# Kernel optimization log

Measured on AMD Instinct MI355X. Metric: run time of the kernel, lower is better.

## Reference

```python
import jax, jax.numpy as jnp
import numpy as np

SEQ, BSZ = 512, 128
VOC, EMB, HDIM = 50000, 128, 256
TAGS = 7
BOS, EOS, PAD = 4, 5, 6
H = HDIM // 2  # per-direction hidden size
NEG = -10000.0


def setup_inputs() -> dict:
    key = jax.random.key(0)
    ks = jax.random.split(key, 12)
    s = 0.08  # ~ pytorch default init scale for these sizes
    trans = jax.random.normal(ks[10], (TAGS, TAGS), dtype=jnp.float32)
    # constraints applied in __init__: no transition FROM BOS targets / INTO EOS etc.
    trans = trans.at[BOS, :].set(NEG).at[:, EOS].set(NEG).at[PAD, :].set(0.0)
    return {
        "sen": jax.random.randint(ks[0], (SEQ, BSZ), 0, VOC),                # (S, B) token ids
        "emb": jax.random.normal(ks[1], (VOC, EMB), jnp.float32) * s,        # embedding table
        "Wih_f": jax.random.normal(ks[2], (4 * H, EMB), jnp.float32) * s,    # fwd dir, gates i,f,g,o
        "Whh_f": jax.random.normal(ks[3], (4 * H, H), jnp.float32) * s,
        "b_f": jax.random.normal(ks[4], (4 * H,), jnp.float32) * s,          # b_ih + b_hh fused
        "Wih_b": jax.random.normal(ks[5], (4 * H, EMB), jnp.float32) * s,    # bwd dir
        "Whh_b": jax.random.normal(ks[6], (4 * H, H), jnp.float32) * s,
        "b_b": jax.random.normal(ks[7], (4 * H,), jnp.float32) * s,
        "W_out": jax.random.normal(ks[8], (TAGS, HDIM), jnp.float32) * s,    # hid2tag
        "b_out": jax.random.normal(ks[9], (TAGS,), jnp.float32) * s,
        "trans": trans,                                                      # trans[next, prev]
    }


def _lstm_dir(x, Wih, Whh, b, reverse):
    """Single-direction LSTM over (S, B, E) -> (S, B, H). PyTorch gate order i,f,g,o."""
    xw = jnp.einsum('sbe,ge->sbg', x, Wih) + b  # hoist input projection out of scan

    def step(carry, xt):
        h, c = carry
        g = xt + h @ Whh.T
        i, f, gg, o = jnp.split(g, 4, axis=-1)
        c = jax.nn.sigmoid(f) * c + jax.nn.sigmoid(i) * jnp.tanh(gg)
        h = jax.nn.sigmoid(o) * jnp.tanh(c)
        return (h, c), h

    B = x.shape[1]
    h0 = jnp.zeros((B, H), x.dtype)
    _, hs = jax.lax.scan(step, (h0, h0), xw, reverse=reverse)
    return hs


def reference(sen, emb, Wih_f, Whh_f, b_f, Wih_b, Whh_b, b_b, W_out, b_out, trans):
    # ----- BiLSTM features -----
    x = emb[sen]                                   # (S, B, E)
    hf = _lstm_dir(x, Wih_f, Whh_f, b_f, reverse=False)
    hb = _lstm_dir(x, Wih_b, Whh_b, b_b, reverse=True)
    fts = jnp.concatenate([hf, hb], axis=-1) @ W_out.T + b_out   # (S, B, TAGS)

    # ----- Viterbi decode (batched, one scan over sequence) -----
    B = fts.shape[1]
    fv0 = jnp.full((B, TAGS), NEG, dtype=fts.dtype).at[:, BOS].set(0.0)

    def vstep(fv, ft):
        # scores[b, next, prev] = fv[b, prev] + trans[next, prev]
        scores = fv[:, None, :] + trans[None, :, :]
        bptr = jnp.argmax(scores, axis=2)          # (B, TAGS) best prev per next tag
        fv_new = jnp.max(scores, axis=2) + ft
        return fv_new, bptr

    fv, bptrs = jax.lax.scan(vstep, fv0, fts)      # bptrs: (S, B, TAGS)
    terminal = fv + trans[EOS]                     # (B, TAGS)
    best = jnp.argmax(terminal, axis=1)            # (B,)
    path_score = jnp.take_along_axis(terminal, best[:, None], axis=1)[:, 0]

    def bstep(cur, bptr):
        prev = jnp.take_along_axis(bptr, cur[:, None], axis=1)[:, 0]
        return prev, cur                           # output = tag at this position

    _, tag_seq = jax.lax.scan(bstep, best, bptrs, reverse=True)  # (S, B)
    return path_score, tag_seq
```

## Files before the change

### kernel.cpp

```cpp
#include <hip/hip_runtime.h>
#include <hip/hip_bf16.h>
#include <math.h>

#define SEQ  512
#define BSZ  128
#define EMBD 128
#define H4   512
#define HD   128
#define NTAG 7
#define BOSX 4
#define EOSX 5
#define NEGC (-10000.0f)

typedef _Float16 h2 __attribute__((ext_vector_type(2)));
typedef _Float16 f16x8 __attribute__((ext_vector_type(8)));
typedef float    f32x4 __attribute__((ext_vector_type(4)));

__device__ __forceinline__ float frcp(float x) { return __builtin_amdgcn_rcpf(x); }

__device__ __forceinline__ float fdot2(h2 a, h2 b, float c) {
#if __has_builtin(__builtin_amdgcn_fdot2)
    return __builtin_amdgcn_fdot2(a, b, c, false);
#else
    return c + (float)a.x * (float)b.x + (float)a.y * (float)b.y;
#endif
}

template<int C> __device__ __forceinline__ float dppaddf(float x) {
    const int y = __builtin_amdgcn_update_dpp(0, __builtin_bit_cast(int, x), C, 0xF, 0xF, true);
    return x + __builtin_bit_cast(float, y);
}
template<int C> __device__ __forceinline__ float dppmovf(float x) {
    return __builtin_bit_cast(float,
        __builtin_amdgcn_update_dpp(0, __builtin_bit_cast(int, x), C, 0xF, 0xF, true));
}
template<int C> __device__ __forceinline__ int dppmovi(int x) {
    return __builtin_amdgcn_update_dpp(0, x, C, 0xF, 0xF, true);
}
__device__ __forceinline__ float kreduce4(float x) {
    x = dppaddf<0xB1>(x);
    x = dppaddf<0x4E>(x);
    return x;
}

#define CH_DW  20
#define ROW_DW 80

__device__ __forceinline__ float dot32h(const h2* __restrict__ w, const h2* __restrict__ x) {
    float a = 0.f;
    #pragma unroll
    for (int j = 0; j < 16; ++j) a = fdot2(w[j], x[j], a);
    return a;
}
__device__ __forceinline__ void ldwh(h2* w, const float4* wr) {
    #pragma unroll
    for (int j = 0; j < 8; ++j) {
        const float4 f4 = wr[j];
        h2 a; a.x = (_Float16)f4.x; a.y = (_Float16)f4.y;
        h2 b; b.x = (_Float16)f4.z; b.y = (_Float16)f4.w;
        w[2 * j] = a; w[2 * j + 1] = b;
    }
}
__device__ __forceinline__ void unp16(const uint4* p, h2* x) {
    #pragma unroll
    for (int j = 0; j < 4; ++j) {
        x[4 * j]     = __builtin_bit_cast(h2, p[j].x);
        x[4 * j + 1] = __builtin_bit_cast(h2, p[j].y);
        x[4 * j + 2] = __builtin_bit_cast(h2, p[j].z);
        x[4 * j + 3] = __builtin_bit_cast(h2, p[j].w);
    }
}

__device__ __forceinline__ void step_barrier() {
    __builtin_amdgcn_sched_barrier(0);
    asm volatile("s_waitcnt lgkmcnt(0)" ::: "memory");
    __builtin_amdgcn_s_barrier();
    __builtin_amdgcn_sched_barrier(0);
}

__global__ __launch_bounds__(512) __attribute__((amdgpu_waves_per_eu(1, 2)))
void bilstm_fused(const int* __restrict__ sen, const float* __restrict__ emb,
                  const float* __restrict__ Wih_f, const float* __restrict__ b_f,
                  const float* __restrict__ Wih_b, const float* __restrict__ b_b,
                  const float* __restrict__ Whh_f, const float* __restrict__ Whh_b,
                  const float* __restrict__ W_out,
                  float* __restrict__ eft, float* __restrict__ ebt)
{
    const int tid = threadIdx.x;
    const int wid = tid >> 6;
    const int lane = tid & 63;
    const int k = lane & 3;
    const int m = lane >> 2;
    const int u = wid * 16 + m;
    const bool bk0 = (lane & 1) != 0;
    const bool bk1 = (lane & 2) != 0;
    const int col = lane & 15;
    const int kg  = lane >> 4;
    const int chain = blockIdx.x;
    const int dir = chain & 1;
    const int b = chain >> 1;
    const int t0 = dir ? (SEQ - 1) : 0;
    const int ts = dir ? -1 : 1;

    __shared__ __align__(16) _Float16 xA[2][4][4][16][8];
    __shared__ __align__(16) float zb[2][8][512];
    __shared__ __align__(16) unsigned hdb_u[2 * ROW_DW];

    const float* __restrict__ Wih  = dir ? Wih_b : Wih_f;
    const float* __restrict__ Whh  = dir ? Whh_b : Whh_f;
    const float* __restrict__ bias = dir ? b_b  : b_f;

    h2 whh[4][16], wo[16];
    #pragma unroll
    for (int g = 0; g < 4; ++g)
        ldwh(whh[g], (const float4*)(Whh + (g * HD + u) * HD + k * 32));
    {
        const int mm = (m < NTAG) ? m : 0;
        ldwh(wo, (const float4*)(W_out + mm * 256 + dir * HD + k * 32));
    }
    f16x8 bw[4][4];
    float biasv[4];
    #pragma unroll
    for (int tt = 0; tt < 4; ++tt) {
        const int R = (wid * 4 + tt) * 16 + col;
        const int ug = R >> 2;
        const int gg = R & 3;
        #pragma unroll
        for (int ks = 0; ks < 4; ++ks) {
            const float* src = Wih + (gg * HD + ug) * EMBD + ks * 32 + kg * 8;
            f16x8 v;
            #pragma unroll
            for (int j = 0; j < 8; ++j) v[j] = (_Float16)src[j];
            bw[tt][ks] = v;
        }
        biasv[tt] = bias[gg * HD + ug];
    }

    if (tid < 2 * ROW_DW) hdb_u[tid] = 0u;
    {
        unsigned* p = (unsigned*)xA;
        p[tid] = 0u; p[tid + 512] = 0u; p[tid + 1024] = 0u; p[tid + 1536] = 0u;
    }

    const int srow = wid;
    const int sp = lane;
    float2 sv;
    auto sissue = [&](int w) {
        const int row = w * 8 + srow;
        const int tg = t0 + ts * row;
        const int tok = sen[tg * BSZ + b];
        sv = *(const float2*)(emb + (size_t)tok * EMBD + 2 * sp);
    };
    auto swrite = [&](int buf) {
        h2 t; t.x = (_Float16)sv.x; t.y = (_Float16)sv.y;
        *(unsigned*)&xA[buf][sp >> 4][(sp >> 2) & 3][srow][(sp & 3) * 2]
            = __builtin_bit_cast(unsigned, t);
    };

    auto proj = [&](int bufp, int nb) {
        f16x8 ax[4];
        #pragma unroll
        for (int ks = 0; ks < 4; ++ks)
            ax[ks] = *(const f16x8*)&xA[bufp][ks][kg][col][0];
        f32x4 acc[4];
        #pragma unroll
        for (int tt = 0; tt < 4; ++tt) { acc[tt][0]=0.f; acc[tt][1]=0.f; acc[tt][2]=0.f; acc[tt][3]=0.f; }
        #pragma unroll
        for (int ks = 0; ks < 4; ++ks)
            #pragma unroll
            for (int tt = 0; tt < 4; ++tt)
                acc[tt] = __builtin_amdgcn_mfma_f32_16x16x32_f16(ax[ks], bw[tt][ks], acc[tt], 0, 0, 0);
        if (lane < 32) {
            #pragma unroll
            for (int tt = 0; tt < 4; ++tt)
                #pragma unroll
                for (int r = 0; r < 4; ++r)
                    zb[nb][(lane >> 4) * 4 + r][wid * 64 + tt * 16 + col]
                        = acc[tt][r] + biasv[tt];
        }
    };

    float c = 0.0f, v0 = 0.0f, v1 = 0.0f, v2 = 0.0f, v3 = 0.0f;
    float zqA, zqB;
    float* __restrict__ eX = (dir ? ebt : eft) + (size_t)b * (SEQ * 8);

    sissue(0); swrite(0);
    sissue(1); swrite(1);
    __syncthreads();
    proj(0, 0);
    sissue(2);
    __syncthreads();
    zqA = zb[0][0][wid * 64 + lane];

    for (int base = 0; base < SEQ; base += 8) {
        const int W = base >> 3;
        #pragma unroll
        for (int sl = 0; sl < 8; ++sl) {
            const int s = base + sl;
            const int cur = sl & 1;
            uint4 hpk[4];
            {
                const uint4* hr = (const uint4*)(hdb_u + cur * ROW_DW + k * CH_DW);
                #pragma unroll
                for (int j = 0; j < 4; ++j) hpk[j] = hr[j];
            }
            if (sl == 0) {
                if (base <= SEQ - 24) swrite(W & 1);
                if (base <= SEQ - 32) sissue(W + 3);
                if (W < 63) proj((W & 1) ^ 1, (W & 1) ^ 1);
            }
            const float xq = (sl & 1) ? zqB : zqA;
            if (s + 1 < SEQ) {
                const int nbuf = (sl == 7) ? ((W & 1) ^ 1) : (W & 1);
                const int nsl = (sl + 1) & 7;
                const float zn = zb[nbuf][nsl][wid * 64 + lane];
                if (sl & 1) zqA = zn; else zqB = zn;
            }
            h2 hx[16];
            unp16(hpk, hx);
            {
                const float pi = dot32h(whh[0], hx);
                const float pf = dot32h(whh[1], hx);
                const float pg = dot32h(whh[2], hx);
                const float po = dot32h(whh[3], hx);
                const float A = (bk0 ? pf : pi) + dppmovf<0xB1>(bk0 ? pi : pf);
                const float B = (bk0 ? po : pg) + dppmovf<0x4E>(bk0 ? pg : po);
                float z = (bk1 ? B : A) + dppmovf<0x4E>(bk1 ? A : B);
                z += xq;
                const bool isg = bk1 && !bk0;
                const float x2 = isg ? (z + z) : z;
                float y = frcp(1.0f + __expf(-x2));
                y = isg ? (2.0f * y - 1.0f) : y;
                const float r1 = dppmovf<0xB1>(y);
                const float r2 = dppmovf<0x4E>(y);
                const float r3 = dppmovf<0x4E>(r1);
                const float i0 = bk0 ? r1 : y,  i1 = bk0 ? y : r1;
                const float i2 = bk0 ? r3 : r2, i3 = bk0 ? r2 : r3;
                const float gi = bk1 ? i2 : i0;
                const float gf = bk1 ? i3 : i1;
                const float gg2 = bk1 ? i0 : i2;
                const float go = bk1 ? i1 : i3;
                c = gf * c + gi * gg2;
                const float th = 2.0f * frcp(1.0f + __expf(-2.0f * c)) - 1.0f;
                const float h = go * th;
                if (k == 0) {
                    ((unsigned short*)hdb_u)[((cur ^ 1) * ROW_DW + (u >> 5) * CH_DW) * 2 + (u & 31)]
                        = __builtin_bit_cast(unsigned short, (_Float16)h);
                }
            }
            if (wid == 0 && s >= 1) {
                const float ev = kreduce4(dot32h(wo, hx));
                const int e = s - 1;
                const bool mine = (e & 3) == k;
                const int j = (e >> 2) & 3;
                v0 = (mine && j == 0) ? ev : v0;
                v1 = (mine && j == 1) ? ev : v1;
                v2 = (mine && j == 2) ? ev : v2;
                v3 = (mine && j == 3) ? ev : v3;
                if ((s & 15) == 0 && m < NTAG) {
                    const int eA = s - 16 + k;
                    eX[(t0 + ts * (eA +  0)) * 8 + m] = v0;
                    eX[(t0 + ts * (eA +  4)) * 8 + m] = v1;
                    eX[(t0 + ts * (eA +  8)) * 8 + m] = v2;
                    eX[(t0 + ts * (eA + 12)) * 8 + m] = v3;
                }
            }
            step_barrier();
        }
    }

    {
        h2 hx[16];
        const uint4* hr = (const uint4*)(hdb_u + k * CH_DW);
        uint4 pk[4];
        #pragma unroll
        for (int j = 0; j < 4; ++j) pk[j] = hr[j];
        unp16(pk, hx);
        if (wid == 0) {
            const float ev = kreduce4(dot32h(wo, hx));
            if (k == 3) v3 = ev;
            if (m < NTAG) {
                const int eA = SEQ - 16 + k;
                eX[(t0 + ts * (eA +  0)) * 8 + m] = v0;
                eX[(t0 + ts * (eA +  4)) * 8 + m] = v1;
                eX[(t0 + ts * (eA +  8)) * 8 + m] = v2;
                eX[(t0 + ts * (eA + 12)) * 8 + m] = v3;
            }
        }
    }
}

__global__ __launch_bounds__(256, 1)
void vit_kernel(const float* __restrict__ eft, const float* __restrict__ ebt,
                const float* __restrict__ b_out, const float* __restrict__ trans,
                float* __restrict__ out)
{
    const int b = blockIdx.x;
    const int tid = threadIdx.x;
    __shared__ __align__(16) float ftl[SEQ * 8];
    __shared__ unsigned wordL[SEQ];

    {
        const float4* sf = (const float4*)(eft + (size_t)b * (SEQ * 8));
        const float4* sb = (const float4*)(ebt + (size_t)b * (SEQ * 8));
        float4* dst = (float4*)ftl;
        #pragma unroll
        for (int i = 0; i < SEQ * 2 / 256; ++i) {
            const int idx = tid + i * 256;
            float4 a = sf[idx];
            const float4 c4 = sb[idx];
            a.x += c4.x; a.y += c4.y; a.z += c4.z; a.w += c4.w;
            dst[idx] = a;
        }
    }
    __syncthreads();

    if (tid < 64) {
        const int lane = tid;
        const int next = lane >> 3;
        const int prev = lane & 7;
        const bool pv = (prev < NTAG);
        const bool nv = (next < NTAG);
        const float trv = (pv && nv) ? (trans[next * NTAG + prev] + b_out[next]) : -3.0e38f;
        float fvp = pv ? ((prev == BOSX) ? 0.0f : NEGC) : -3.0e38f;

        for (int t = 0; t < SEQ; ++t) {
            float mv = fvp + trv;
            int am = prev;
            {
                const float om = dppmovf<0xB1>(mv); const int oa = dppmovi<0xB1>(am);
                if (om > mv || (om == mv && oa < am)) { mv = om; am = oa; }
            }
            {
                const float om = dppmovf<0x4E>(mv); const int oa = dppmovi<0x4E>(am);
                if (om > mv || (om == mv && oa < am)) { mv = om; am = oa; }
            }
            {
                const float om = dppmovf<0x141>(mv); const int oa = dppmovi<0x141>(am);
                if (om > mv || (om == mv && oa < am)) { mv = om; am = oa; }
            }
            const float fvnew = mv + ftl[t * 8 + next];
            const float nfv = __shfl(fvnew, (lane & 7) << 3);
            const int   amg = __shfl(am,    (lane & 7) << 3);
            unsigned pw = (unsigned)amg << (3 * prev);
            pw |= (unsigned)dppmovi<0xB1>((int)pw);
            pw |= (unsigned)dppmovi<0x4E>((int)pw);
            pw |= (unsigned)dppmovi<0x141>((int)pw);
            if (lane == 0) wordL[t] = pw;
            fvp = pv ? nfv : -3.0e38f;
        }

        float term = pv ? (fvp + trans[EOSX * NTAG + prev]) : -3.0e38f;
        int am = prev;
        {
            const float om = dppmovf<0xB1>(term); const int oa = dppmovi<0xB1>(am);
            if (om > term || (om == term && oa < am)) { term = om; am = oa; }
        }
        {
            const float om = dppmovf<0x4E>(term); const int oa = dppmovi<0x4E>(am);
            if (om > term || (om == term && oa < am)) { term = om; am = oa; }
        }
        {
            const float om = dppmovf<0x141>(term); const int oa = dppmovi<0x141>(am);
            if (om > term || (om == term && oa < am)) { term = om; am = oa; }
        }
        if (lane == 0) out[b] = term;

        unsigned wd[8];
        #pragma unroll
        for (int c2 = 0; c2 < 8; ++c2) wd[c2] = wordL[c2 * 64 + lane];
        int cur = __builtin_amdgcn_readfirstlane(am);
        unsigned pr[8];
        #pragma unroll
        for (int c2 = 7; c2 >= 0; --c2) {
            unsigned acc = 0u;
            for (int tt = 63; tt >= 0; --tt) {
                acc = (lane == tt) ? (unsigned)cur : acc;
                const unsigned w = (unsigned)__builtin_amdgcn_readlane((int)wd[c2], tt);
                cur = (int)((w >> (3 * cur)) & 7u);
            }
            pr[c2] = acc;
        }
        #pragma unroll
        for (int c2 = 0; c2 < 8; ++c2)
            out[BSZ + (c2 * 64 + lane) * BSZ + b] = (float)pr[c2];
    }
}

extern "C" void kernel_launch(void* const* d_in, const int* in_sizes, int n_in,
                              void* d_out, int out_size, void* d_ws, size_t ws_size,
                              hipStream_t stream)
{
    const int*   sen   = (const int*)d_in[0];
    const float* emb   = (const float*)d_in[1];
    const float* Wih_f = (const float*)d_in[2];
    const float* Whh_f = (const float*)d_in[3];
    const float* b_f   = (const float*)d_in[4];
    const float* Wih_b = (const float*)d_in[5];
    const float* Whh_b = (const float*)d_in[6];
    const float* b_b   = (const float*)d_in[7];
    const float* W_out = (const float*)d_in[8];
    const float* b_out = (const float*)d_in[9];
    const float* trans = (const float*)d_in[10];
    float* out = (float*)d_out;

    char* ws = (char*)d_ws;
    const size_t ft_bytes = (size_t)BSZ * SEQ * 8 * 4;
    float* eft = (float*)ws;
    float* ebt = (float*)(ws + ft_bytes);

    bilstm_fused<<<dim3(2 * BSZ), dim3(512), 0, stream>>>(
        sen, emb, Wih_f, b_f, Wih_b, b_b, Whh_f, Whh_b, W_out, eft, ebt);
    vit_kernel<<<dim3(BSZ), dim3(256), 0, stream>>>(eft, ebt, b_out, trans, out);
}
```

Before: 554.2 us.

## Split LSTM recurrence across 1024 threads with 8-way k reduction

Doubles the block size of the fused BiLSTM kernel from 512 to 1024 threads. Each hidden unit's recurrent dot products are now split over 8 lanes of 16 elements instead of 4 lanes of 32, and a third DPP shuffle stage completes the reduction. The input projection tiles are halved per wave, and the hidden-state buffer becomes a plain fp16 array. The aim is to shorten the per-step serial latency of the recurrence, at the cost of more waves per barrier, extra DPP work, and the register cap set by waves_per_eu(4,4).

Result: slower. 615.9 us (+11.1%).

```diff
diff --git a/kernel.cpp b/kernel.cpp
--- a/kernel.cpp
+++ b/kernel.cpp
@@ -5,7 +5,6 @@
 #define SEQ  512
 #define BSZ  128
 #define EMBD 128
-#define H4   512
 #define HD   128
 #define NTAG 7
 #define BOSX 4
@@ -37,33 +36,30 @@
 template<int C> __device__ __forceinline__ int dppmovi(int x) {
     return __builtin_amdgcn_update_dpp(0, x, C, 0xF, 0xF, true);
 }
-__device__ __forceinline__ float kreduce4(float x) {
+__device__ __forceinline__ float kreduce8(float x) {
     x = dppaddf<0xB1>(x);
     x = dppaddf<0x4E>(x);
-    return x;
-}
-
-#define CH_DW  20
-#define ROW_DW 80
-
-__device__ __forceinline__ float dot32h(const h2* __restrict__ w, const h2* __restrict__ x) {
+    return x + dppmovf<0x141>(x);
+}
+
+__device__ __forceinline__ float dot16h(const h2* __restrict__ w, const h2* __restrict__ x) {
     float a = 0.f;
     #pragma unroll
-    for (int j = 0; j < 16; ++j) a = fdot2(w[j], x[j], a);
+    for (int j = 0; j < 8; ++j) a = fdot2(w[j], x[j], a);
     return a;
 }
-__device__ __forceinline__ void ldwh(h2* w, const float4* wr) {
+__device__ __forceinline__ void ldwh8(h2* w, const float4* wr) {
     #pragma unroll
-    for (int j = 0; j < 8; ++j) {
+    for (int j = 0; j < 4; ++j) {
         const float4 f4 = wr[j];
         h2 a; a.x = (_Float16)f4.x; a.y = (_Float16)f4.y;
         h2 b; b.x = (_Float16)f4.z; b.y = (_Float16)f4.w;
         w[2 * j] = a; w[2 * j + 1] = b;
     }
 }
-__device__ __forceinline__ void unp16(const uint4* p, h2* x) {
+__device__ __forceinline__ void unp8(const uint4* p, h2* x) {
     #pragma unroll
-    for (int j = 0; j < 4; ++j) {
+    for (int j = 0; j < 2; ++j) {
         x[4 * j]     = __builtin_bit_cast(h2, p[j].x);
         x[4 * j + 1] = __builtin_bit_cast(h2, p[j].y);
         x[4 * j + 2] = __builtin_bit_cast(h2, p[j].z);
@@ -78,7 +74,7 @@
     __builtin_amdgcn_sched_barrier(0);
 }
 
-__global__ __launch_bounds__(512) __attribute__((amdgpu_waves_per_eu(1, 2)))
+__global__ __launch_bounds__(1024) __attribute__((amdgpu_waves_per_eu(4, 4)))
 void bilstm_fused(const int* __restrict__ sen, const float* __restrict__ emb,
                   const float* __restrict__ Wih_f, const float* __restrict__ b_f,
                   const float* __restrict__ Wih_b, const float* __restrict__ b_b,
@@ -89,11 +85,13 @@
     const int tid = threadIdx.x;
     const int wid = tid >> 6;
     const int lane = tid & 63;
-    const int k = lane & 3;
-    const int m = lane >> 2;
-    const int u = wid * 16 + m;
+    const int k8 = lane & 7;
+    const int m8 = lane >> 3;
+    const int q  = lane & 3;
+    const int u  = wid * 8 + m8;
     const bool bk0 = (lane & 1) != 0;
     const bool bk1 = (lane & 2) != 0;
+    const bool bk2 = (lane & 4) != 0;
     const int col = lane & 15;
     const int kg  = lane >> 4;
     const int chain = blockIdx.x;
@@ -104,25 +102,26 @@
 
     __shared__ __align__(16) _Float16 xA[2][4][4][16][8];
     __shared__ __align__(16) float zb[2][8][512];
-    __shared__ __align__(16) unsigned hdb_u[2 * ROW_DW];
+    __shared__ __align__(16) _Float16 hdb[2][128];
 
     const float* __restrict__ Wih  = dir ? Wih_b : Wih_f;
     const float* __restrict__ Whh  = dir ? Whh_b : Whh_f;
     const float* __restrict__ bias = dir ? b_b  : b_f;
 
-    h2 whh[4][16], wo[16];
+    h2 whh[4][8];
     #pragma unroll
     for (int g = 0; g < 4; ++g)
-        ldwh(whh[g], (const float4*)(Whh + (g * HD + u) * HD + k * 32));
+        ldwh8(whh[g], (const float4*)(Whh + (g * HD + u) * HD + k8 * 16));
+    h2 wo[8];
     {
-        const int mm = (m < NTAG) ? m : 0;
-        ldwh(wo, (const float4*)(W_out + mm * 256 + dir * HD + k * 32));
-    }
-    f16x8 bw[4][4];
-    float biasv[4];
+        const int mm = (m8 < NTAG) ? m8 : 0;
+        ldwh8(wo, (const float4*)(W_out + mm * 256 + dir * HD + k8 * 16));
+    }
+    f16x8 bw[2][4];
+    float biasv[2];
     #pragma unroll
-    for (int tt = 0; tt < 4; ++tt) {
-        const int R = (wid * 4 + tt) * 16 + col;
+    for (int tt = 0; tt < 2; ++tt) {
+        const int R = (wid * 2 + tt) * 16 + col;
         const int ug = R >> 2;
         const int gg = R & 3;
         #pragma unroll
@@ -136,22 +135,24 @@
         biasv[tt] = bias[gg * HD + ug];
     }
 
-    if (tid < 2 * ROW_DW) hdb_u[tid] = 0u;
+    if (tid < 128) ((unsigned*)hdb)[tid] = 0u;
     {
         unsigned* p = (unsigned*)xA;
-        p[tid] = 0u; p[tid + 512] = 0u; p[tid + 1024] = 0u; p[tid + 1536] = 0u;
+        p[tid] = 0u; p[tid + 1024] = 0u;
     }
 
     const int srow = wid;
     const int sp = lane;
     float2 sv;
     auto sissue = [&](int w) {
+        if (wid >= 8) return;
         const int row = w * 8 + srow;
         const int tg = t0 + ts * row;
         const int tok = sen[tg * BSZ + b];
         sv = *(const float2*)(emb + (size_t)tok * EMBD + 2 * sp);
     };
     auto swrite = [&](int buf) {
+        if (wid >= 8) return;
         h2 t; t.x = (_Float16)sv.x; t.y = (_Float16)sv.y;
         *(unsigned*)&xA[buf][sp >> 4][(sp >> 2) & 3][srow][(sp & 3) * 2]
             = __builtin_bit_cast(unsigned, t);
@@ -162,27 +163,28 @@
         #pragma unroll
         for (int ks = 0; ks < 4; ++ks)
             ax[ks] = *(const f16x8*)&xA[bufp][ks][kg][col][0];
-        f32x4 acc[4];
-        #pragma unroll
-        for (int tt = 0; tt < 4; ++tt) { acc[tt][0]=0.f; acc[tt][1]=0.f; acc[tt][2]=0.f; acc[tt][3]=0.f; }
+        f32x4 acc[2];
+        #pragma unroll
+        for (int tt = 0; tt < 2; ++tt) { acc[tt][0]=0.f; acc[tt][1]=0.f; acc[tt][2]=0.f; acc[tt][3]=0.f; }
         #pragma unroll
         for (int ks = 0; ks < 4; ++ks)
             #pragma unroll
-            for (int tt = 0; tt < 4; ++tt)
+            for (int tt = 0; tt < 2; ++tt)
                 acc[tt] = __builtin_amdgcn_mfma_f32_16x16x32_f16(ax[ks], bw[tt][ks], acc[tt], 0, 0, 0);
         if (lane < 32) {
             #pragma unroll
-            for (int tt = 0; tt < 4; ++tt)
+            for (int tt = 0; tt < 2; ++tt)
                 #pragma unroll
                 for (int r = 0; r < 4; ++r)
-                    zb[nb][(lane >> 4) * 4 + r][wid * 64 + tt * 16 + col]
+                    zb[nb][(lane >> 4) * 4 + r][wid * 32 + tt * 16 + col]
                         = acc[tt][r] + biasv[tt];
         }
     };
 
-    float c = 0.0f, v0 = 0.0f, v1 = 0.0f, v2 = 0.0f, v3 = 0.0f;
+    float c = 0.0f, v0 = 0.0f, v1 = 0.0f;
     float zqA, zqB;
     float* __restrict__ eX = (dir ? ebt : eft) + (size_t)b * (SEQ * 8);
+    const int zrow = wid * 32 + m8 * 4 + q;
 
     sissue(0); swrite(0);
     sissue(1); swrite(1);
@@ -190,7 +192,7 @@
     proj(0, 0);
     sissue(2);
     __syncthreads();
-    zqA = zb[0][0][wid * 64 + lane];
+    zqA = zb[0][0][zrow];
 
     for (int base = 0; base < SEQ; base += 8) {
         const int W = base >> 3;
@@ -198,11 +200,10 @@
         for (int sl = 0; sl < 8; ++sl) {
             const int s = base + sl;
             const int cur = sl & 1;
-            uint4 hpk[4];
+            uint4 hpk[2];
             {
-                const uint4* hr = (const uint4*)(hdb_u + cur * ROW_DW + k * CH_DW);
-                #pragma unroll
-                for (int j = 0; j < 4; ++j) hpk[j] = hr[j];
+                const uint4* hr = (const uint4*)&hdb[cur][k8 * 16];
+                hpk[0] = hr[0]; hpk[1] = hr[1];
             }
             if (sl == 0) {
                 if (base <= SEQ - 24) swrite(W & 1);
@@ -213,20 +214,21 @@
             if (s + 1 < SEQ) {
                 const int nbuf = (sl == 7) ? ((W & 1) ^ 1) : (W & 1);
                 const int nsl = (sl + 1) & 7;
-                const float zn = zb[nbuf][nsl][wid * 64 + lane];
+                const float zn = zb[nbuf][nsl][zrow];
                 if (sl & 1) zqA = zn; else zqB = zn;
             }
-            h2 hx[16];
-            unp16(hpk, hx);
+            h2 hx[8];
+            unp8(hpk, hx);
             {
-                const float pi = dot32h(whh[0], hx);
-                const float pf = dot32h(whh[1], hx);
-                const float pg = dot32h(whh[2], hx);
-                const float po = dot32h(whh[3], hx);
+                const float pi = dot16h(whh[0], hx);
+                const float pf = dot16h(whh[1], hx);
+                const float pg = dot16h(whh[2], hx);
+                const float po = dot16h(whh[3], hx);
                 const float A = (bk0 ? pf : pi) + dppmovf<0xB1>(bk0 ? pi : pf);
-                const float B = (bk0 ? po : pg) + dppmovf<0x4E>(bk0 ? pg : po);
-                float z = (bk1 ? B : A) + dppmovf<0x4E>(bk1 ? A : B);
-                z += xq;
+                const float B = (bk0 ? po : pg) + dppmovf<0xB1>(bk0 ? pg : po);
+                const float z1 = (bk1 ? B : A) + dppmovf<0x4E>(bk1 ? A : B);
+                const float zs = bk2 ? dppmovf<0x104>(z1) : dppmovf<0x114>(z1);
+                float z = z1 + zs + xq;
                 const bool isg = bk1 && !bk0;
                 const float x2 = isg ? (z + z) : z;
                 float y = frcp(1.0f + __expf(-x2));
@@ -243,49 +245,38 @@
                 c = gf * c + gi * gg2;
                 const float th = 2.0f * frcp(1.0f + __expf(-2.0f * c)) - 1.0f;
                 const float h = go * th;
-                if (k == 0) {
-                    ((unsigned short*)hdb_u)[((cur ^ 1) * ROW_DW + (u >> 5) * CH_DW) * 2 + (u & 31)]
-                        = __builtin_bit_cast(unsigned short, (_Float16)h);
-                }
+                if (k8 == 0)
+                    hdb[cur ^ 1][u] = (_Float16)h;
             }
             if (wid == 0 && s >= 1) {
-                const float ev = kreduce4(dot32h(wo, hx));
+                const float ev = kreduce8(dot16h(wo, hx));
                 const int e = s - 1;
-                const bool mine = (e & 3) == k;
-                const int j = (e >> 2) & 3;
+                const bool mine = (e & 7) == k8;
+                const int j = (e >> 3) & 1;
                 v0 = (mine && j == 0) ? ev : v0;
                 v1 = (mine && j == 1) ? ev : v1;
-                v2 = (mine && j == 2) ? ev : v2;
-                v3 = (mine && j == 3) ? ev : v3;
-                if ((s & 15) == 0 && m < NTAG) {
-                    const int eA = s - 16 + k;
-                    eX[(t0 + ts * (eA +  0)) * 8 + m] = v0;
-                    eX[(t0 + ts * (eA +  4)) * 8 + m] = v1;
-                    eX[(t0 + ts * (eA +  8)) * 8 + m] = v2;
-                    eX[(t0 + ts * (eA + 12)) * 8 + m] = v3;
+                if ((s & 15) == 0 && m8 < NTAG) {
+                    const int eA = s - 16 + k8;
+                    eX[(t0 + ts * (eA + 0)) * 8 + m8] = v0;
+                    eX[(t0 + ts * (eA + 8)) * 8 + m8] = v1;
                 }
             }
             step_barrier();
         }
     }
 
-    {
-        h2 hx[16];
-        const uint4* hr = (const uint4*)(hdb_u + k * CH_DW);
-        uint4 pk[4];
-        #pragma unroll
-        for (int j = 0; j < 4; ++j) pk[j] = hr[j];
-        unp16(pk, hx);
-        if (wid == 0) {
-            const float ev = kreduce4(dot32h(wo, hx));
-            if (k == 3) v3 = ev;
-            if (m < NTAG) {
-                const int eA = SEQ - 16 + k;
-                eX[(t0 + ts * (eA +  0)) * 8 + m] = v0;
-                eX[(t0 + ts * (eA +  4)) * 8 + m] = v1;
-                eX[(t0 + ts * (eA +  8)) * 8 + m] = v2;
-                eX[(t0 + ts * (eA + 12)) * 8 + m] = v3;
-            }
+    if (wid == 0) {
+        uint4 hpk[2];
+        const uint4* hr = (const uint4*)&hdb[0][k8 * 16];
+        hpk[0] = hr[0]; hpk[1] = hr[1];
+        h2 hx[8];
+        unp8(hpk, hx);
+        const float ev = kreduce8(dot16h(wo, hx));
+        if (k8 == 7) v1 = ev;
+        if (m8 < NTAG) {
+            const int eA = SEQ - 16 + k8;
+            eX[(t0 + ts * (eA + 0)) * 8 + m8] = v0;
+            eX[(t0 + ts * (eA + 8)) * 8 + m8] = v1;
         }
     }
 }
@@ -409,7 +400,7 @@
     float* eft = (float*)ws;
     float* ebt = (float*)(ws + ft_bytes);
 
-    bilstm_fused<<<dim3(2 * BSZ), dim3(512), 0, stream>>>(
+    bilstm_fused<<<dim3(2 * BSZ), dim3(1024), 0, stream>>>(
         sen, emb, Wih_f, b_f, Wih_b, b_b, Whh_f, Whh_b, W_out, eft, ebt);
     vit_kernel<<<dim3(BSZ), dim3(256), 0, stream>>>(eft, ebt, b_out, trans, out);
 }
```
